# Performance work log

Measured on AMD Instinct MI355X. Metric: run time of the kernel, lower is better.

The kernel has to match this reference:

```python
import jax, jax.numpy as jnp
import numpy as np

N, C_IN, C_OUT, T, V = 64, 64, 64, 300, 25
INTER_C = C_OUT // 4
NUM_SUBSET = 3
BN_EPS = 1e-5


def setup_inputs() -> dict:
    key = jax.random.key(0)
    ks = jax.random.split(key, 12)
    w_scale = 0.05  # keep attention logits in a sane range
    return {
        "x": jax.random.normal(ks[0], (N, C_IN, T, V), jnp.float32),
        "A": jax.random.uniform(ks[1], (NUM_SUBSET, V, V), jnp.float32),
        "graph_attn": jnp.ones((NUM_SUBSET, V, V), jnp.float32),
        "g_w": jax.random.normal(ks[2], (NUM_SUBSET, C_OUT, C_IN), jnp.float32) * w_scale,
        "g_b": jax.random.normal(ks[3], (NUM_SUBSET, C_OUT), jnp.float32) * w_scale,
        "a_w": jax.random.normal(ks[4], (NUM_SUBSET, INTER_C, C_IN), jnp.float32) * w_scale,
        "a_b": jax.random.normal(ks[5], (NUM_SUBSET, INTER_C), jnp.float32) * w_scale,
        "b_w": jax.random.normal(ks[6], (NUM_SUBSET, INTER_C, C_IN), jnp.float32) * w_scale,
        "b_b": jax.random.normal(ks[7], (NUM_SUBSET, INTER_C), jnp.float32) * w_scale,
        "bn_gamma": jax.random.uniform(ks[8], (C_OUT,), jnp.float32, 0.5, 1.5),
        "bn_beta": jax.random.normal(ks[9], (C_OUT,), jnp.float32) * 0.1,
        "bn_mean": jax.random.normal(ks[10], (C_OUT,), jnp.float32) * 0.1,
        "bn_var": jax.random.uniform(ks[11], (C_OUT,), jnp.float32, 0.5, 1.5),
    }


def _conv1x1(x, w, b):
    # 1x1 Conv2d over channel dim of [N, C, T, V]
    return jnp.einsum('nctv,oc->notv', x, w) + b[None, :, None, None]


def reference(x, A, graph_attn, g_w, g_b, a_w, a_b, b_w, b_b,
              bn_gamma, bn_beta, bn_mean, bn_var):
    A_full = A + graph_attn  # [3, V, V]
    hidden = None
    for i in range(NUM_SUBSET):
        A1 = _conv1x1(x, a_w[i], a_b[i]).transpose(0, 3, 1, 2)  # [N, V, inter_c, T]
        A2 = _conv1x1(x, b_w[i], b_b[i])                        # [N, inter_c, T, V]
        # [N, V, W, T] attention logits, softmax over axis -2 (W)
        S = jnp.einsum('nvct,nctw->nvwt', A1, A2) / INTER_C
        S = jax.nn.softmax(S, axis=-2)
        S = S + A_full[i][None, :, :, None]
        # faithful to torch: sum S over its first spatial axis, elementwise on x
        z = _conv1x1(jnp.einsum('nctv,nwvt->nctv', x, S), g_w[i], g_b[i])
        hidden = z if hidden is None else hidden + z
    # inference-mode BatchNorm2d
    inv = jax.lax.rsqrt(bn_var + BN_EPS)
    h = (hidden - bn_mean[None, :, None, None]) * (bn_gamma * inv)[None, :, None, None] \
        + bn_beta[None, :, None, None]
    # in_channels == out_channels -> identity residual
    h = h + x
    return jax.nn.relu(h)
```

## Files before the change

kernel.cpp:

```cpp
#include <hip/hip_runtime.h>
#include <hip/hip_bf16.h>
#include <math.h>


typedef __attribute__((ext_vector_type(8)))  short bf8;
typedef __attribute__((ext_vector_type(4)))  short bf4;
typedef __attribute__((ext_vector_type(4)))  float f4;
typedef __attribute__((ext_vector_type(16))) float f16v;

#define TT     2
#define COLS   50
#define XROW   72
#define PQROW  40
#define OUTROW 64

#define SM_XB    0
#define SM_PQ    7200
#define SM_COLA  12320
#define SM_SIZE  12624

#define WS_AW    0
#define WS_BW    6144
#define WS_GW    12288
#define WS_COLA  36864
#define WS_SCL   37376
#define WS_SHF   37632
#define WS_END   37888

__device__ __forceinline__ short f2bf(float f) {
  __hip_bfloat16 h = __float2bfloat16(f);
  return __builtin_bit_cast(short, h);
}
__device__ __forceinline__ float bf2f(short s) {
  union { unsigned u; float f; } v;
  v.u = ((unsigned)(unsigned short)s) << 16;
  return v.f;
}
__device__ __forceinline__ float rsum16(float v) {
  v += __shfl_xor(v, 1);
  v += __shfl_xor(v, 2);
  v += __shfl_xor(v, 4);
  v += __shfl_xor(v, 8);
  return v;
}

__global__ void tagc_prep(
    const float* __restrict__ A,    const float* __restrict__ G,
    const float* __restrict__ g_w,  const float* __restrict__ g_b,
    const float* __restrict__ a_w,  const float* __restrict__ b_w,
    const float* __restrict__ bn_g, const float* __restrict__ bn_b,
    const float* __restrict__ bn_m, const float* __restrict__ bn_v,
    short* __restrict__ aw_bf, short* __restrict__ bw_bf,
    short* __restrict__ gw_bf, float* __restrict__ colA3,
    float* __restrict__ scl,   float* __restrict__ shf2)
{
  const int b = blockIdx.x, tid = threadIdx.x;
  if (b < 12) {
    int base = b * 1024 + tid * 4;
    f4 v = *(const f4*)(g_w + base);
    bf4 o;
    #pragma unroll
    for (int r = 0; r < 4; ++r) o[r] = f2bf(v[r]);
    *(bf4*)(gw_bf + base) = o;
  } else if (b == 12) {
    #pragma unroll
    for (int g = 0; g < 3; ++g) {
      int base = g * 1024 + tid * 4;
      f4 v = *(const f4*)(a_w + base);
      bf4 o;
      #pragma unroll
      for (int r = 0; r < 4; ++r) o[r] = f2bf(v[r]);
      *(bf4*)(aw_bf + base) = o;
    }
  } else if (b == 13) {
    #pragma unroll
    for (int g = 0; g < 3; ++g) {
      int base = g * 1024 + tid * 4;
      f4 v = *(const f4*)(b_w + base);
      bf4 o;
      #pragma unroll
      for (int r = 0; r < 4; ++r) o[r] = f2bf(v[r]);
      *(bf4*)(bw_bf + base) = o;
    }
  } else if (b == 14) {
    if (tid < 75) {
      int i = tid / 25, v = tid - 25 * i;
      float s = 0.f;
      for (int a = 0; a < 25; ++a)
        s += A[i * 625 + a * 25 + v] + G[i * 625 + a * 25 + v];
      colA3[tid] = s;
    }
  } else {
    if (tid < 64) {
      float sc  = bn_g[tid] * rsqrtf(bn_v[tid] + 1e-5f);
      float gbs = g_b[tid] + g_b[64 + tid] + g_b[128 + tid];
      scl[tid]  = sc;
      shf2[tid] = bn_b[tid] - bn_m[tid] * sc + gbs * sc;
    }
  }
}

__launch_bounds__(128, 4)
__global__ void tagc_v10_kernel(
    const float* __restrict__ x,
    const float* __restrict__ a_b,
    const float* __restrict__ b_b,
    const short* __restrict__ aw_bf,
    const short* __restrict__ bw_bf,
    const short* __restrict__ gw_bf,
    const float* __restrict__ colA3,
    const float* __restrict__ sclp,
    const float* __restrict__ shf2p,
    float* __restrict__ out)
{
  __shared__ __align__(16) char smem[SM_SIZE];
  short* Xb   = (short*)(smem + SM_XB);
  short* PQs  = (short*)(smem + SM_PQ);
  float* colA = (float*)(smem + SM_COLA);
  float* OutS = (float*)smem;

  const int tid  = threadIdx.x;
  const int wave = tid >> 6;
  const int lane = tid & 63;
  const int l15  = lane & 15;
  const int quad = lane >> 4;
  const int l31  = lane & 31;
  const int hl   = lane >> 5;

  const int lin = blockIdx.y * 150 + blockIdx.x;
  const int idx = lin >> 3;
  const int n   = ((lin & 7) << 3) + idx / 150;
  const int t0  = (idx % 150) * TT;

  if (tid < 75) colA[tid] = colA3[tid];

  {
    const float* xb = x + (long)n * 480000 + t0 * 25;
    #pragma unroll
    for (int k = 0; k < 7; ++k) {
      int idxs = k * 128 + tid;
      if (idxs < 800) {
        int c4  = idxs / 50;
        int col = idxs - 50 * c4;
        bf4 wv;
        #pragma unroll
        for (int j = 0; j < 4; ++j)
          wv[j] = f2bf(xb[(4 * c4 + j) * 7500 + col]);
        *(bf4*)&Xb[col * XROW + 4 * c4] = wv;
      }
    }
  }

  f16v R0, R1;
  #pragma unroll
  for (int r = 0; r < 16; ++r) { R0[r] = 0.f; R1[r] = 0.f; }

  __syncthreads();

  const int w25 = wave * 25;
  short* PQw = PQs + wave * (32 * PQROW);
  const bf8 Z8 = {0,0,0,0,0,0,0,0};

  for (int i = 0; i < 3; ++i) {
    #pragma unroll
    for (int mt = 0; mt < 2; ++mt) {
      const short* Wb = (mt ? bw_bf : aw_bf) + i * 1024;
      const float* Bv = (mt ? b_b : a_b) + i * 16;
      bf8 W0 = *(const bf8*)(Wb + l15 * 64 + quad * 8);
      bf8 W1 = *(const bf8*)(Wb + l15 * 64 + 32 + quad * 8);
      float b0 = Bv[quad * 4 + 0], b1 = Bv[quad * 4 + 1];
      float b2 = Bv[quad * 4 + 2], b3 = Bv[quad * 4 + 3];
      #pragma unroll
      for (int ct = 0; ct < 2; ++ct) {
        bf8 B0 = Z8, B1 = Z8;
        if (ct == 0 || l15 < 9) {
          int row = w25 + ct * 16 + l15;
          B0 = *(const bf8*)&Xb[row * XROW + quad * 8];
          B1 = *(const bf8*)&Xb[row * XROW + 32 + quad * 8];
        }
        f4 acc = {0.f, 0.f, 0.f, 0.f};
        acc = __builtin_amdgcn_mfma_f32_16x16x32_bf16(W0, B0, acc, 0, 0, 0);
        acc = __builtin_amdgcn_mfma_f32_16x16x32_bf16(W1, B1, acc, 0, 0, 0);
        bf4 pw;
        pw[0] = f2bf(acc[0] + b0); pw[1] = f2bf(acc[1] + b1);
        pw[2] = f2bf(acc[2] + b2); pw[3] = f2bf(acc[3] + b3);
        *(bf4*)&PQw[(ct * 16 + l15) * PQROW + mt * 16 + quad * 4] = pw;
      }
    }

    bf8 Bq0 = Z8, Bq1 = Z8;
    if (quad < 2)
      Bq0 = *(const bf8*)&PQw[l15 * PQROW + 16 + quad * 8];
    if (quad < 2 && l15 < 9)
      Bq1 = *(const bf8*)&PQw[(16 + l15) * PQROW + 16 + quad * 8];
    const bool w1ok = (l15 < 9);
    float cs0 = 0.f, cs1 = 0.f;
    #pragma unroll
    for (int am = 0; am < 2; ++am) {
      bf8 Afr = Z8;
      if (quad < 2 && (am * 16 + l15) < 25)
        Afr = *(const bf8*)&PQw[(am * 16 + l15) * PQROW + quad * 8];
      f4 z0 = {0.f, 0.f, 0.f, 0.f};
      f4 z1 = {0.f, 0.f, 0.f, 0.f};
      z0 = __builtin_amdgcn_mfma_f32_16x16x32_bf16(Afr, Bq0, z0, 0, 0, 0);
      z1 = __builtin_amdgcn_mfma_f32_16x16x32_bf16(Afr, Bq1, z1, 0, 0, 0);
      #pragma unroll
      for (int r = 0; r < 4; ++r) {
        float e0 = __expf(z0[r] * 0.0625f);
        float e1 = w1ok ? __expf(z1[r] * 0.0625f) : 0.f;
        float d  = rsum16(e0 + e1);
        float rd = 1.f / d;
        int a = am * 16 + quad * 4 + r;
        if (a < 25) { cs0 += e0 * rd; cs1 += e1 * rd; }
      }
    }
    cs0 += __shfl_xor(cs0, 16); cs0 += __shfl_xor(cs0, 32);
    cs1 += __shfl_xor(cs1, 16); cs1 += __shfl_xor(cs1, 32);
    float sval = 0.f;
    if (l31 < 25) {
      float csel = (l31 < 16) ? cs0 : cs1;
      sval = csel + colA[i * 25 + l31];
    }

    #pragma unroll
    for (int tr = 0; tr < 2; ++tr) {
      f16v za;
      #pragma unroll
      for (int r = 0; r < 16; ++r) za[r] = 0.f;
      #pragma unroll
      for (int kk = 0; kk < 4; ++kk) {
        bf8 Bf = Z8;
        if (l31 < 25)
          Bf = *(const bf8*)&Xb[(w25 + l31) * XROW + kk * 16 + hl * 8];
        bf8 Ag = *(const bf8*)(gw_bf + i * 4096 + (tr * 32 + l31) * 64 + kk * 16 + hl * 8);
        za = __builtin_amdgcn_mfma_f32_32x32x16_bf16(Ag, Bf, za, 0, 0, 0);
      }
      if (tr == 0) {
        #pragma unroll
        for (int r = 0; r < 16; ++r) R0[r] += za[r] * sval;
      } else {
        #pragma unroll
        for (int r = 0; r < 16; ++r) R1[r] += za[r] * sval;
      }
    }
  }

  if (l31 < 25) {
    const int col = w25 + l31;
    #pragma unroll
    for (int tr = 0; tr < 2; ++tr) {
      #pragma unroll
      for (int rg = 0; rg < 4; ++rg) {
        int ob = tr * 32 + rg * 8 + hl * 4;
        f4 sc = *(const f4*)(sclp + ob);
        f4 sh = *(const f4*)(shf2p + ob);
        bf4 res = *(const bf4*)&Xb[col * XROW + ob];
        #pragma unroll
        for (int r = 0; r < 4; ++r) {
          float acc = tr ? R1[rg * 4 + r] : R0[rg * 4 + r];
          float hv = fmaxf(acc * sc[r] + sh[r] + bf2f(res[r]), 0.f);
          if (tr) R1[rg * 4 + r] = hv; else R0[rg * 4 + r] = hv;
        }
      }
    }
  }

  __syncthreads();

  float* obase = out + (long)n * 480000 + t0 * 25;
  #pragma unroll
  for (int ro = 0; ro < 2; ++ro) {
    if (ro) __syncthreads();
    if (l31 < 25) {
      const int col = w25 + l31;
      #pragma unroll
      for (int rg = 0; rg < 4; ++rg) {
        int lr = rg * 8 + hl * 4;
        #pragma unroll
        for (int r = 0; r < 4; ++r)
          OutS[(lr + r) * OUTROW + col] = ro ? R1[rg * 4 + r] : R0[rg * 4 + r];
      }
    }
    __syncthreads();
    #pragma unroll
    for (int it = 0; it < 4; ++it) {
      int idx2 = it * 128 + tid;
      int lr = idx2 >> 4, ch = idx2 & 15;
      if (ch < 12) {
        f4 vv = *(const f4*)&OutS[lr * OUTROW + ch * 4];
        *(f4*)(obase + (long)(ro * 32 + lr) * 7500 + ch * 4) = vv;
      }
    }
    if (tid < 32) {
      float2 vv = *(const float2*)&OutS[tid * OUTROW + 48];
      *(float2*)(obase + (long)(ro * 32 + tid) * 7500 + 48) = vv;
    }
  }
}

extern "C" void kernel_launch(void* const* d_in, const int* in_sizes, int n_in,
                              void* d_out, int out_size, void* d_ws, size_t ws_size,
                              hipStream_t stream) {
  (void)in_sizes; (void)n_in; (void)ws_size; (void)out_size;
  char* ws = (char*)d_ws;
  short* aw_bf = (short*)(ws + WS_AW);
  short* bw_bf = (short*)(ws + WS_BW);
  short* gw_bf = (short*)(ws + WS_GW);
  float* colA3 = (float*)(ws + WS_COLA);
  float* scl   = (float*)(ws + WS_SCL);
  float* shf2  = (float*)(ws + WS_SHF);

  tagc_prep<<<dim3(16), dim3(256), 0, stream>>>(
      (const float*)d_in[1],  (const float*)d_in[2],
      (const float*)d_in[3],  (const float*)d_in[4],
      (const float*)d_in[5],  (const float*)d_in[7],
      (const float*)d_in[9],  (const float*)d_in[10],
      (const float*)d_in[11], (const float*)d_in[12],
      aw_bf, bw_bf, gw_bf, colA3, scl, shf2);

  dim3 grid(300 / TT, 64);
  tagc_v10_kernel<<<grid, dim3(128), 0, stream>>>(
      (const float*)d_in[0],
      (const float*)d_in[6],  (const float*)d_in[8],
      aw_bf, bw_bf, gw_bf, colA3, scl, shf2,
      (float*)d_out);
}
```

Before: 334.9 us.

## Restructure subset loop into phases with hoisted X fragments and per-subset PQ buffers

The X fragments used by the A/B projections and by the g-conv MFMAs are now loaded once into registers and reused across all three subsets, instead of being reloaded from LDS each iteration. The single subset loop is split into three phases: projections for all subsets, softmax column sums for all subsets, then the g-conv accumulation. This needs separate PQ scratch per subset, which grows shared memory from about 12.6KB to 19.5KB. The aim is fewer LDS reads and more independent MFMA work for the scheduler, at the cost of higher register pressure and LDS footprint under launch_bounds(128,4).

```diff
diff --git a/kernel.cpp b/kernel.cpp
--- a/kernel.cpp
+++ b/kernel.cpp
@@ -12,12 +12,13 @@
 #define COLS   50
 #define XROW   72
 #define PQROW  40
+#define PQSUB  (25 * PQROW)
 #define OUTROW 64
 
 #define SM_XB    0
 #define SM_PQ    7200
-#define SM_COLA  12320
-#define SM_SIZE  12624
+#define SM_COLA  19200
+#define SM_SIZE  19504
 
 #define WS_AW    0
 #define WS_BW    6144
@@ -101,7 +102,7 @@
 }
 
 __launch_bounds__(128, 4)
-__global__ void tagc_v10_kernel(
+__global__ void tagc_v11_kernel(
     const float* __restrict__ x,
     const float* __restrict__ a_b,
     const float* __restrict__ b_b,
@@ -151,17 +152,27 @@
     }
   }
 
-  f16v R0, R1;
-  #pragma unroll
-  for (int r = 0; r < 16; ++r) { R0[r] = 0.f; R1[r] = 0.f; }
-
   __syncthreads();
 
   const int w25 = wave * 25;
-  short* PQw = PQs + wave * (32 * PQROW);
+  short* PQw = PQs + wave * (3 * PQSUB);
   const bf8 Z8 = {0,0,0,0,0,0,0,0};
 
+  bf8 XA00, XA01, XA10 = Z8, XA11 = Z8;
+  {
+    int row0 = (w25 + l15) * XROW;
+    XA00 = *(const bf8*)&Xb[row0 + quad * 8];
+    XA01 = *(const bf8*)&Xb[row0 + 32 + quad * 8];
+    if (l15 < 9) {
+      int row1 = (w25 + 16 + l15) * XROW;
+      XA10 = *(const bf8*)&Xb[row1 + quad * 8];
+      XA11 = *(const bf8*)&Xb[row1 + 32 + quad * 8];
+    }
+  }
+
+  #pragma unroll
   for (int i = 0; i < 3; ++i) {
+    short* Pi = PQw + i * PQSUB;
     #pragma unroll
     for (int mt = 0; mt < 2; ++mt) {
       const short* Wb = (mt ? bw_bf : aw_bf) + i * 1024;
@@ -170,36 +181,45 @@
       bf8 W1 = *(const bf8*)(Wb + l15 * 64 + 32 + quad * 8);
       float b0 = Bv[quad * 4 + 0], b1 = Bv[quad * 4 + 1];
       float b2 = Bv[quad * 4 + 2], b3 = Bv[quad * 4 + 3];
-      #pragma unroll
-      for (int ct = 0; ct < 2; ++ct) {
-        bf8 B0 = Z8, B1 = Z8;
-        if (ct == 0 || l15 < 9) {
-          int row = w25 + ct * 16 + l15;
-          B0 = *(const bf8*)&Xb[row * XROW + quad * 8];
-          B1 = *(const bf8*)&Xb[row * XROW + 32 + quad * 8];
-        }
+      {
         f4 acc = {0.f, 0.f, 0.f, 0.f};
-        acc = __builtin_amdgcn_mfma_f32_16x16x32_bf16(W0, B0, acc, 0, 0, 0);
-        acc = __builtin_amdgcn_mfma_f32_16x16x32_bf16(W1, B1, acc, 0, 0, 0);
+        acc = __builtin_amdgcn_mfma_f32_16x16x32_bf16(W0, XA00, acc, 0, 0, 0);
+        acc = __builtin_amdgcn_mfma_f32_16x16x32_bf16(W1, XA01, acc, 0, 0, 0);
         bf4 pw;
         pw[0] = f2bf(acc[0] + b0); pw[1] = f2bf(acc[1] + b1);
         pw[2] = f2bf(acc[2] + b2); pw[3] = f2bf(acc[3] + b3);
-        *(bf4*)&PQw[(ct * 16 + l15) * PQROW + mt * 16 + quad * 4] = pw;
-      }
-    }
-
+        *(bf4*)&Pi[l15 * PQROW + mt * 16 + quad * 4] = pw;
+      }
+      {
+        f4 acc = {0.f, 0.f, 0.f, 0.f};
+        acc = __builtin_amdgcn_mfma_f32_16x16x32_bf16(W0, XA10, acc, 0, 0, 0);
+        acc = __builtin_amdgcn_mfma_f32_16x16x32_bf16(W1, XA11, acc, 0, 0, 0);
+        if (l15 < 9) {
+          bf4 pw;
+          pw[0] = f2bf(acc[0] + b0); pw[1] = f2bf(acc[1] + b1);
+          pw[2] = f2bf(acc[2] + b2); pw[3] = f2bf(acc[3] + b3);
+          *(bf4*)&Pi[(16 + l15) * PQROW + mt * 16 + quad * 4] = pw;
+        }
+      }
+    }
+  }
+
+  float svals[3];
+  #pragma unroll
+  for (int i = 0; i < 3; ++i) {
+    const short* Pi = PQw + i * PQSUB;
     bf8 Bq0 = Z8, Bq1 = Z8;
     if (quad < 2)
-      Bq0 = *(const bf8*)&PQw[l15 * PQROW + 16 + quad * 8];
+      Bq0 = *(const bf8*)&Pi[l15 * PQROW + 16 + quad * 8];
     if (quad < 2 && l15 < 9)
-      Bq1 = *(const bf8*)&PQw[(16 + l15) * PQROW + 16 + quad * 8];
+      Bq1 = *(const bf8*)&Pi[(16 + l15) * PQROW + 16 + quad * 8];
     const bool w1ok = (l15 < 9);
     float cs0 = 0.f, cs1 = 0.f;
     #pragma unroll
     for (int am = 0; am < 2; ++am) {
       bf8 Afr = Z8;
       if (quad < 2 && (am * 16 + l15) < 25)
-        Afr = *(const bf8*)&PQw[(am * 16 + l15) * PQROW + quad * 8];
+        Afr = *(const bf8*)&Pi[(am * 16 + l15) * PQROW + quad * 8];
       f4 z0 = {0.f, 0.f, 0.f, 0.f};
       f4 z1 = {0.f, 0.f, 0.f, 0.f};
       z0 = __builtin_amdgcn_mfma_f32_16x16x32_bf16(Afr, Bq0, z0, 0, 0, 0);
@@ -221,26 +241,39 @@
       float csel = (l31 < 16) ? cs0 : cs1;
       sval = csel + colA[i * 25 + l31];
     }
-
+    svals[i] = sval;
+  }
+
+  f16v R0, R1;
+  #pragma unroll
+  for (int r = 0; r < 16; ++r) { R0[r] = 0.f; R1[r] = 0.f; }
+
+  bf8 Bf0 = Z8, Bf1 = Z8, Bf2 = Z8, Bf3 = Z8;
+  if (l31 < 25) {
+    int rb = (w25 + l31) * XROW + hl * 8;
+    Bf0 = *(const bf8*)&Xb[rb];
+    Bf1 = *(const bf8*)&Xb[rb + 16];
+    Bf2 = *(const bf8*)&Xb[rb + 32];
+    Bf3 = *(const bf8*)&Xb[rb + 48];
+  }
+  #pragma unroll
+  for (int i = 0; i < 3; ++i) {
     #pragma unroll
     for (int tr = 0; tr < 2; ++tr) {
+      const short* gp = gw_bf + i * 4096 + (tr * 32 + l31) * 64 + hl * 8;
       f16v za;
       #pragma unroll
       for (int r = 0; r < 16; ++r) za[r] = 0.f;
-      #pragma unroll
-      for (int kk = 0; kk < 4; ++kk) {
-        bf8 Bf = Z8;
-        if (l31 < 25)
-          Bf = *(const bf8*)&Xb[(w25 + l31) * XROW + kk * 16 + hl * 8];
-        bf8 Ag = *(const bf8*)(gw_bf + i * 4096 + (tr * 32 + l31) * 64 + kk * 16 + hl * 8);
-        za = __builtin_amdgcn_mfma_f32_32x32x16_bf16(Ag, Bf, za, 0, 0, 0);
-      }
+      za = __builtin_amdgcn_mfma_f32_32x32x16_bf16(*(const bf8*)(gp),      Bf0, za, 0, 0, 0);
+      za = __builtin_amdgcn_mfma_f32_32x32x16_bf16(*(const bf8*)(gp + 16), Bf1, za, 0, 0, 0);
+      za = __builtin_amdgcn_mfma_f32_32x32x16_bf16(*(const bf8*)(gp + 32), Bf2, za, 0, 0, 0);
+      za = __builtin_amdgcn_mfma_f32_32x32x16_bf16(*(const bf8*)(gp + 48), Bf3, za, 0, 0, 0);
       if (tr == 0) {
         #pragma unroll
-        for (int r = 0; r < 16; ++r) R0[r] += za[r] * sval;
+        for (int r = 0; r < 16; ++r) R0[r] += za[r] * svals[i];
       } else {
         #pragma unroll
-        for (int r = 0; r < 16; ++r) R1[r] += za[r] * sval;
+        for (int r = 0; r < 16; ++r) R1[r] += za[r] * svals[i];
       }
     }
   }
@@ -319,7 +352,7 @@
       aw_bf, bw_bf, gw_bf, colA3, scl, shf2);
 
   dim3 grid(300 / TT, 64);
-  tagc_v10_kernel<<<grid, dim3(128), 0, stream>>>(
+  tagc_v11_kernel<<<grid, dim3(128), 0, stream>>>(
       (const float*)d_in[0],
       (const float*)d_in[6],  (const float*)d_in[8],
       aw_bf, bw_bf, gw_bf, colA3, scl, shf2,
```

Result: no change. 339.8 us (+1.5%).

## Enlarge block to 10 time steps with 10 waves and swizzled LDS X tile

Applied to the files above, without the earlier changes.

Each block now covers 10 time steps (250 columns) with 10 waves instead of 2 time steps with 2 waves, so blocks are fewer and larger. The X tile row pitch drops from 72 to 64 shorts with an XOR swizzle to avoid LDS bank conflicts, and the output staging is rewritten with contiguous float2 stores across the wider tile. PQ stores for out-of-range rows are now skipped. LDS use grows to about 52KB per block, which limits how many blocks fit per CU.

```diff
diff --git a/kernel.cpp b/kernel.cpp
--- a/kernel.cpp
+++ b/kernel.cpp
@@ -6,18 +6,21 @@
 typedef __attribute__((ext_vector_type(8)))  short bf8;
 typedef __attribute__((ext_vector_type(4)))  short bf4;
 typedef __attribute__((ext_vector_type(4)))  float f4;
+typedef __attribute__((ext_vector_type(2)))  float f2;
 typedef __attribute__((ext_vector_type(16))) float f16v;
 
-#define TT     2
-#define COLS   50
-#define XROW   72
+#define TT     10
+#define NW     10
+#define COLS   250
+#define XROW   64
 #define PQROW  40
-#define OUTROW 64
+#define PQSUB  (25 * PQROW)
+#define OUTROW 250
 
 #define SM_XB    0
-#define SM_PQ    7200
-#define SM_COLA  12320
-#define SM_SIZE  12624
+#define SM_PQ    32000
+#define SM_COLA  52000
+#define SM_SIZE  52304
 
 #define WS_AW    0
 #define WS_BW    6144
@@ -42,6 +45,9 @@
   v += __shfl_xor(v, 4);
   v += __shfl_xor(v, 8);
   return v;
+}
+__device__ __forceinline__ int xsw(int row, int sh) {
+  return row * XROW + (sh ^ ((row & 7) << 3));
 }
 
 __global__ void tagc_prep(
@@ -100,8 +106,8 @@
   }
 }
 
-__launch_bounds__(128, 4)
-__global__ void tagc_v10_kernel(
+__launch_bounds__(640, 6)
+__global__ void tagc_v12_kernel(
     const float* __restrict__ x,
     const float* __restrict__ a_b,
     const float* __restrict__ b_b,
@@ -127,10 +133,10 @@
   const int l31  = lane & 31;
   const int hl   = lane >> 5;
 
-  const int lin = blockIdx.y * 150 + blockIdx.x;
+  const int lin = blockIdx.y * 30 + blockIdx.x;
   const int idx = lin >> 3;
-  const int n   = ((lin & 7) << 3) + idx / 150;
-  const int t0  = (idx % 150) * TT;
+  const int n   = ((lin & 7) << 3) + idx / 30;
+  const int t0  = (idx % 30) * TT;
 
   if (tid < 75) colA[tid] = colA3[tid];
 
@@ -138,15 +144,15 @@
     const float* xb = x + (long)n * 480000 + t0 * 25;
     #pragma unroll
     for (int k = 0; k < 7; ++k) {
-      int idxs = k * 128 + tid;
-      if (idxs < 800) {
-        int c4  = idxs / 50;
-        int col = idxs - 50 * c4;
+      int idxs = k * 640 + tid;
+      if (idxs < 4000) {
+        int c4  = idxs / 250;
+        int col = idxs - 250 * c4;
         bf4 wv;
         #pragma unroll
         for (int j = 0; j < 4; ++j)
           wv[j] = f2bf(xb[(4 * c4 + j) * 7500 + col]);
-        *(bf4*)&Xb[col * XROW + 4 * c4] = wv;
+        *(bf4*)&Xb[xsw(col, 4 * c4)] = wv;
       }
     }
   }
@@ -158,7 +164,7 @@
   __syncthreads();
 
   const int w25 = wave * 25;
-  short* PQw = PQs + wave * (32 * PQROW);
+  short* PQw = PQs + wave * PQSUB;
   const bf8 Z8 = {0,0,0,0,0,0,0,0};
 
   for (int i = 0; i < 3; ++i) {
@@ -175,16 +181,18 @@
         bf8 B0 = Z8, B1 = Z8;
         if (ct == 0 || l15 < 9) {
           int row = w25 + ct * 16 + l15;
-          B0 = *(const bf8*)&Xb[row * XROW + quad * 8];
-          B1 = *(const bf8*)&Xb[row * XROW + 32 + quad * 8];
+          B0 = *(const bf8*)&Xb[xsw(row, quad * 8)];
+          B1 = *(const bf8*)&Xb[xsw(row, 32 + quad * 8)];
         }
         f4 acc = {0.f, 0.f, 0.f, 0.f};
         acc = __builtin_amdgcn_mfma_f32_16x16x32_bf16(W0, B0, acc, 0, 0, 0);
         acc = __builtin_amdgcn_mfma_f32_16x16x32_bf16(W1, B1, acc, 0, 0, 0);
-        bf4 pw;
-        pw[0] = f2bf(acc[0] + b0); pw[1] = f2bf(acc[1] + b1);
-        pw[2] = f2bf(acc[2] + b2); pw[3] = f2bf(acc[3] + b3);
-        *(bf4*)&PQw[(ct * 16 + l15) * PQROW + mt * 16 + quad * 4] = pw;
+        if (ct == 0 || l15 < 9) {
+          bf4 pw;
+          pw[0] = f2bf(acc[0] + b0); pw[1] = f2bf(acc[1] + b1);
+          pw[2] = f2bf(acc[2] + b2); pw[3] = f2bf(acc[3] + b3);
+          *(bf4*)&PQw[(ct * 16 + l15) * PQROW + mt * 16 + quad * 4] = pw;
+        }
       }
     }
 
@@ -231,7 +239,7 @@
       for (int kk = 0; kk < 4; ++kk) {
         bf8 Bf = Z8;
         if (l31 < 25)
-          Bf = *(const bf8*)&Xb[(w25 + l31) * XROW + kk * 16 + hl * 8];
+          Bf = *(const bf8*)&Xb[xsw(w25 + l31, kk * 16 + hl * 8)];
         bf8 Ag = *(const bf8*)(gw_bf + i * 4096 + (tr * 32 + l31) * 64 + kk * 16 + hl * 8);
         za = __builtin_amdgcn_mfma_f32_32x32x16_bf16(Ag, Bf, za, 0, 0, 0);
       }
@@ -254,7 +262,7 @@
         int ob = tr * 32 + rg * 8 + hl * 4;
         f4 sc = *(const f4*)(sclp + ob);
         f4 sh = *(const f4*)(shf2p + ob);
-        bf4 res = *(const bf4*)&Xb[col * XROW + ob];
+        bf4 res = *(const bf4*)&Xb[xsw(col, ob)];
         #pragma unroll
         for (int r = 0; r < 4; ++r) {
           float acc = tr ? R1[rg * 4 + r] : R0[rg * 4 + r];
@@ -283,17 +291,13 @@
     }
     __syncthreads();
     #pragma unroll
-    for (int it = 0; it < 4; ++it) {
-      int idx2 = it * 128 + tid;
-      int lr = idx2 >> 4, ch = idx2 & 15;
-      if (ch < 12) {
-        f4 vv = *(const f4*)&OutS[lr * OUTROW + ch * 4];
-        *(f4*)(obase + (long)(ro * 32 + lr) * 7500 + ch * 4) = vv;
-      }
-    }
-    if (tid < 32) {
-      float2 vv = *(const float2*)&OutS[tid * OUTROW + 48];
-      *(float2*)(obase + (long)(ro * 32 + tid) * 7500 + 48) = vv;
+    for (int it = 0; it < 7; ++it) {
+      int idx2 = it * 640 + tid;
+      if (idx2 < 4000) {
+        int lr = idx2 / 125, ch = idx2 - 125 * lr;
+        f2 vv = *(const f2*)&OutS[lr * OUTROW + ch * 2];
+        *(f2*)(obase + (long)(ro * 32 + lr) * 7500 + ch * 2) = vv;
+      }
     }
   }
 }
@@ -319,7 +323,7 @@
       aw_bf, bw_bf, gw_bf, colA3, scl, shf2);
 
   dim3 grid(300 / TT, 64);
-  tagc_v10_kernel<<<grid, dim3(128), 0, stream>>>(
+  tagc_v12_kernel<<<grid, dim3(640), 0, stream>>>(
       (const float*)d_in[0],
       (const float*)d_in[6],  (const float*)d_in[8],
       aw_bf, bw_bf, gw_bf, colA3, scl, shf2,
```

New measurement: 484.3 us. +44.6%, slower.
